# Optimization experiments

Hardware: AMD Instinct MI355X
Metric: run time of the kernel (lower is better)

## Reference

```python
import math
import jax, jax.numpy as jnp
import numpy as np

B, N, D = 64, 1024, 512


def setup_inputs() -> dict:
    key = jax.random.key(0)
    k1, k2, k3 = jax.random.split(key, 3)
    x = jax.random.normal(k1, (B, N, D), dtype=jnp.float32)
    # non-padded-elements mask: True = valid object (all valid here so every
    # softmax row has finite entries despite the -inf self-mask on the diagonal)
    mask = jnp.ones((B, N), dtype=bool)
    # fc_out = nn.Linear(D, D): weight [D, D] (out, in) and bias [D]
    lim = 1.0 / math.sqrt(D)
    W = jax.random.uniform(k2, (D, D), dtype=jnp.float32, minval=-lim, maxval=lim)
    b = jax.random.uniform(k3, (D,), dtype=jnp.float32, minval=-lim, maxval=lim)
    return {"x": x, "mask": mask, "W": W, "b": b}


def reference(x, mask, W, b):
    bsz, max_objs, embed_dim = x.shape
    xs = x / math.sqrt(embed_dim)  # note: values are the scaled x too (as in torch code)
    # sims[b, i, j] = <xs[b,i], xs[b,j]>
    sims = jnp.einsum('bid,bjd->bij', xs, xs)
    # mask padded KEYS (columns): ~mask -> -inf
    sims = jnp.where(mask[:, None, :], sims, -jnp.inf)
    # self-exclusion: eye(N).fill_diagonal_(-inf) == -inf on diag, 0 off-diag
    self_mask = jnp.where(jnp.eye(max_objs, dtype=bool), -jnp.inf, 0.0).astype(sims.dtype)
    sims = sims + self_mask
    attn_weights = jax.nn.softmax(sims, axis=-1)
    attn = jnp.einsum('bij,bjd->bid', attn_weights, xs)
    out = attn @ W.T + b
    return out
```

## Files before the change

kernel.cpp:

```cpp
#include <hip/hip_runtime.h>
#include <hip/hip_bf16.h>
#include <cstdint>
#include <cstddef>


typedef float f32x4 __attribute__((ext_vector_type(4)));
typedef unsigned short ushort4v __attribute__((ext_vector_type(4)));
typedef long longx2 __attribute__((ext_vector_type(2)));

#if __has_builtin(__builtin_amdgcn_cvt_pk_fp8_f32)
static __device__ __forceinline__ unsigned pk4_fp8(float a, float b, float c,
                                                   float d) {
  unsigned u = (unsigned)__builtin_amdgcn_cvt_pk_fp8_f32(a, b, 0, false);
  u = (unsigned)__builtin_amdgcn_cvt_pk_fp8_f32(c, d, (int)u, true);
  return u;
}
#else
static __device__ __forceinline__ unsigned f2e4m3_sw(float f) {
  unsigned s = (__float_as_uint(f) >> 24) & 0x80u;
  float a = fabsf(f);
  if (a != a) return s | 0x7fu;
  if (a > 448.f) a = 448.f;
  if (a == 0.f) return s;
  int e;
  float m = frexpf(a, &e);
  if (e - 1 < -6) {
    unsigned q = (unsigned)rintf(a * 512.f);
    return s | q;
  }
  unsigned q = (unsigned)rintf(m * 16.f);
  if (q == 16u) { q = 8u; e += 1; }
  return s | ((unsigned)(e - 1 + 7) << 3) | (q - 8u);
}
static __device__ __forceinline__ unsigned pk4_fp8(float a, float b, float c,
                                                   float d) {
  return f2e4m3_sw(a) | (f2e4m3_sw(b) << 8) | (f2e4m3_sw(c) << 16) |
         (f2e4m3_sw(d) << 24);
}
#endif

static __device__ __forceinline__ int perm8(int k) {
  return (k & ~127) | (k & 64) | (((k >> 3) & 3) << 4) |
         (((k >> 5) & 1) << 3) | (k & 7);
}

#define GLDS16(src, dst)                                                        \
  __builtin_amdgcn_global_load_lds(                                             \
      (const __attribute__((address_space(1))) void*)(src),                     \
      (__attribute__((address_space(3))) void*)(dst), 16, 0, 0)

__global__ __launch_bounds__(256) void convert_kernel(
    const float* __restrict__ x, unsigned char* __restrict__ xf8,
    unsigned char* __restrict__ xT8, const float* __restrict__ W,
    unsigned char* __restrict__ W8) {
  const int bid = blockIdx.x;
  const int t = threadIdx.x;
  if (bid >= 8192) {
    const int f0 = ((bid - 8192) * 256 + t) * 4;
    const int row = f0 >> 9, col = f0 & 511;
    const float4 v = *(const float4*)(W + f0);
    const unsigned u =
        pk4_fp8(v.x * 8.f, v.y * 8.f, v.z * 8.f, v.w * 8.f);
    *(unsigned*)(W8 + (size_t)row * 512 + perm8(col)) = u;
    return;
  }
  const int b = bid >> 7;
  const int tile = bid & 127;
  const int n0 = (tile >> 3) * 64;
  const int d0 = (tile & 7) * 64;
  __shared__ unsigned char T8[64][80];
  const float sc = 0.04419417382415922f;
  const size_t xbase = ((size_t)b * 1024 + n0) * 512 + d0;
#pragma unroll
  for (int q = 0; q < 2; ++q) {
    const int u = q * 256 + t;
    const int r = u >> 3, j = u & 7;
    const float4 v0 = *(const float4*)(x + xbase + (size_t)r * 512 + j * 8);
    const float4 v1 = *(const float4*)(x + xbase + (size_t)r * 512 + j * 8 + 4);
    const unsigned lo = pk4_fp8(v0.x * sc, v0.y * sc, v0.z * sc, v0.w * sc);
    const unsigned hi = pk4_fp8(v1.x * sc, v1.y * sc, v1.z * sc, v1.w * sc);
    const unsigned long long pk =
        (unsigned long long)lo | ((unsigned long long)hi << 32);
    const int k = d0 + j * 8;
    *(unsigned long long*)(xf8 + ((size_t)b * 1024 + n0 + r) * 512 +
                           perm8(k)) = pk;
    *(unsigned long long*)(&T8[r][j * 8]) = pk;
  }
  __syncthreads();
  const int dd = t >> 2;
  const int nc0 = (t & 3) * 16;
  unsigned long long lo = 0, hi = 0;
#pragma unroll
  for (int j = 0; j < 8; ++j) {
    lo |= (unsigned long long)T8[nc0 + j][dd] << (8 * j);
    hi |= (unsigned long long)T8[nc0 + 8 + j][dd] << (8 * j);
  }
  const size_t rowb = ((size_t)b * 512 + d0 + dd) * 1024;
  const int gn0 = n0 + nc0;
  *(unsigned long long*)(xT8 + rowb + perm8(gn0)) = lo;
  *(unsigned long long*)(xT8 + rowb + perm8(gn0 + 8)) = hi;
}

__global__ __launch_bounds__(256) void rsum_reduce_kernel(
    const float* __restrict__ part, float* __restrict__ invr) {
  const int i = blockIdx.x * 256 + threadIdx.x;
  const int b = i >> 10, row = i & 1023;
  const float* p = part + (size_t)b * 16384 + row;
  float s = 0.0f;
#pragma unroll
  for (int j = 0; j < 16; ++j) s += p[j * 1024];
  invr[i] = 1.0f / s;
}

template <int KB, int MODE, bool TRI>
__global__ __launch_bounds__(512, 4) void g128_kernel(
    const unsigned char* __restrict__ A, const unsigned char* __restrict__ Bm,
    void* __restrict__ Out, float* __restrict__ aux, int mB, int nB,
    size_t aBatch, size_t bBatch, size_t oBatch, int aStride, int bStride,
    int oStride) {
  __shared__ __align__(16) unsigned char lds[73728];

  const int nwg = gridDim.x;
  int bid = blockIdx.x;
  {
    const int xcd = bid & 7, loc = bid >> 3;
    const int q = nwg >> 3, r8 = nwg & 7;
    bid = (xcd < r8 ? xcd * (q + 1) : r8 * (q + 1) + (xcd - r8) * q) + loc;
  }
  int pb, mb, nb;
  if (TRI) {
    pb = bid / 20;
    int r = bid - pb * 20;
    mb = 0;
    while (r >= 8 - 2 * mb) { r -= 8 - 2 * mb; ++mb; }
    nb = 2 * mb + r;
  } else {
    const int per = mB * nB;
    pb = bid / per;
    const int rem = bid - pb * per;
    mb = rem / nB;
    nb = rem - mb * nB;
  }

  const int t = threadIdx.x;
  const int lane = t & 63;
  const int w = t >> 6;
  const int wm = w >> 1;
  const int wn = w & 1;
  const int g = lane >> 4, cc = lane & 15;

  const unsigned char* Ab =
      A + (size_t)pb * aBatch + (size_t)(mb * 256) * aStride;
  const unsigned char* Bb =
      Bm + (size_t)pb * bBatch + (size_t)(nb * 128) * bStride;

  const int rowS = t >> 2;
  const int swc = (((t & 3) ^ ((rowS >> 1) & 3)) << 4);

  auto stageA = [&](int slot, int half, int kt) {
    const unsigned char* src =
        Ab + (size_t)(half * 128 + rowS) * aStride + kt * 64 + swc;
    GLDS16(src, lds + slot * 16384 + half * 8192 + t * 16);
  };
  auto stageB = [&](int slot, int kt) {
    const unsigned char* src = Bb + (size_t)rowS * bStride + kt * 64 + swc;
    GLDS16(src, lds + 49152 + slot * 8192 + t * 16);
  };

  const int swz = ((g ^ ((cc >> 1) & 3)) << 4);
  const int aBase = wm * 4096 + cc * 64 + swz;
  const int bBase = wn * 4096 + cc * 64 + swz;

  f32x4 acc[4][4];
#pragma unroll
  for (int mt = 0; mt < 4; ++mt)
#pragma unroll
    for (int nt = 0; nt < 4; ++nt) acc[mt][nt] = 0.0f;

  longx2 af[4], bv[4];

  auto readAf = [&](int slot) {
#pragma unroll
    for (int j = 0; j < 4; ++j)
      af[j] = *reinterpret_cast<const longx2*>(lds + slot * 16384 + aBase +
                                               j * 1024);
  };
  auto readBf = [&](int slot) {
#pragma unroll
    for (int n = 0; n < 4; ++n)
      bv[n] = *reinterpret_cast<const longx2*>(lds + 49152 + slot * 8192 +
                                               bBase + n * 1024);
  };
  auto mfmaH = [&](int nh) {
    __builtin_amdgcn_s_setprio(1);
#pragma unroll
    for (int j = 0; j < 4; ++j)
#pragma unroll
      for (int n = 0; n < 2; ++n) {
        acc[j][nh * 2 + n] = __builtin_amdgcn_mfma_f32_16x16x32_fp8_fp8(
            bv[nh * 2 + n][0], af[j][0], acc[j][nh * 2 + n], 0, 0, 0);
        acc[j][nh * 2 + n] = __builtin_amdgcn_mfma_f32_16x16x32_fp8_fp8(
            bv[nh * 2 + n][1], af[j][1], acc[j][nh * 2 + n], 0, 0, 0);
      }
    __builtin_amdgcn_s_setprio(0);
  };

  stageA(0, 0, 0);
  stageA(0, 1, 0);
  stageB(0, 0);
  stageA(1, 0, 1);
  stageA(1, 1, 1);
  stageB(1, 1);
  asm volatile("s_waitcnt vmcnt(3)" ::: "memory");
  __builtin_amdgcn_s_barrier();

  int sl = 0;
#pragma unroll 1
  for (int kt = 0; kt < KB; ++kt) {
    const int s2 = (sl >= 1) ? sl - 1 : 2;
    const bool pf = (kt + 2 < KB);
    readAf(sl);
    readBf(sl);
    if (pf) {
      stageA(s2, 0, kt + 2);
      stageA(s2, 1, kt + 2);
      stageB(s2, kt + 2);
    }
    mfmaH(0);
    mfmaH(1);
    if (pf)
      asm volatile("s_waitcnt vmcnt(3)" ::: "memory");
    else
      asm volatile("s_waitcnt vmcnt(0)" ::: "memory");
    __builtin_amdgcn_s_barrier();
    sl = (sl == 2) ? 0 : sl + 1;
  }

  if (MODE == 0) {
    unsigned char* P = (unsigned char*)Out + (size_t)pb * oBatch;
    const bool mir = TRI && (nb >= 2 * mb + 2);
    float rs[4];
    float cs[4][4];
#pragma unroll
    for (int mt = 0; mt < 4; ++mt) rs[mt] = 0.0f;
#pragma unroll
    for (int nt = 0; nt < 4; ++nt)
#pragma unroll
      for (int r = 0; r < 4; ++r) cs[nt][r] = 0.0f;
#pragma unroll
    for (int mt = 0; mt < 4; ++mt) {
      const int ml = wm * 64 + mt * 16 + cc;
      const int mm = mb * 256 + ml;
#pragma unroll
      for (int nt = 0; nt < 4; ++nt) {
        const int cb = nb * 128 + wn * 64 + nt * 16 + g * 4;
        float p[4];
#pragma unroll
        for (int r = 0; r < 4; ++r) {
          p[r] = (mm == cb + r) ? 0.0f : __expf(acc[mt][nt][r]);
          rs[mt] += p[r];
        }
        const unsigned u = pk4_fp8(p[0], p[1], p[2], p[3]);
        *(unsigned*)(P + (size_t)mm * oStride + perm8(cb)) = u;
        if (mir) {
#pragma unroll
          for (int r = 0; r < 4; ++r) {
            const int nl = wn * 64 + nt * 16 + g * 4 + r;
            lds[nl * 256 + (ml ^ ((nl & 7) << 4))] =
                (unsigned char)(u >> (8 * r));
            cs[nt][r] += p[r];
          }
        }
      }
    }
#pragma unroll
    for (int mt = 0; mt < 4; ++mt) {
      rs[mt] += __shfl_xor(rs[mt], 16);
      rs[mt] += __shfl_xor(rs[mt], 32);
    }
    if (lane < 16) {
      const int sm = TRI ? (nb - 2 * mb) * 2 + wn : nb * 2 + wn;
      float* prt = aux + ((size_t)pb * 16 + sm) * 1024;
#pragma unroll
      for (int mt = 0; mt < 4; ++mt)
        prt[mb * 256 + wm * 64 + mt * 16 + lane] = rs[mt];
    }
    if (mir) {
#pragma unroll
      for (int nt = 0; nt < 4; ++nt)
#pragma unroll
        for (int r = 0; r < 4; ++r) {
          float v = cs[nt][r];
          v += __shfl_xor(v, 1);
          v += __shfl_xor(v, 2);
          v += __shfl_xor(v, 4);
          v += __shfl_xor(v, 8);
          if (cc == 0) {
            const int n = wn * 64 + nt * 16 + g * 4 + r;
            aux[((size_t)pb * 16 + (12 - 4 * mb + wm)) * 1024 + nb * 128 +
                n] = v;
          }
        }
      __syncthreads();
      const int nl = t >> 2, q4 = t & 3;
      const int swn = (nl & 7) << 4;
      unsigned char* Pm =
          P + (size_t)(nb * 128 + nl) * oStride + mb * 256;
#pragma unroll
      for (int c = 0; c < 4; ++c) {
        const int mc = q4 * 64 + c * 16;
        const unsigned long long* src =
            (const unsigned long long*)(lds + nl * 256 + (mc ^ swn));
        const unsigned long long q0 = src[0], q1 = src[1];
        *(unsigned long long*)(Pm + perm8(mc)) = q0;
        *(unsigned long long*)(Pm + perm8(mc + 8)) = q1;
      }
    }
  } else if (MODE == 1) {
    unsigned char* Ao = (unsigned char*)Out + (size_t)pb * oBatch;
    const float* invr = aux;
#pragma unroll
    for (int mt = 0; mt < 4; ++mt) {
      const int mm = mb * 256 + wm * 64 + mt * 16 + cc;
      const float inv = invr[(size_t)pb * 1024 + mm] * 256.0f;
#pragma unroll
      for (int nt = 0; nt < 4; ++nt) {
        const int nn = nb * 128 + wn * 64 + nt * 16 + g * 4;
        *(unsigned*)(Ao + (size_t)mm * oStride + perm8(nn)) =
            pk4_fp8(acc[mt][nt][0] * inv, acc[mt][nt][1] * inv,
                    acc[mt][nt][2] * inv, acc[mt][nt][3] * inv);
      }
    }
  } else {
    float* O = (float*)Out;
    const float* bias = (const float*)aux;
    const float is = 1.0f / 2048.0f;
#pragma unroll
    for (int mt = 0; mt < 4; ++mt) {
      const int mm = mb * 256 + wm * 64 + mt * 16 + cc;
#pragma unroll
      for (int nt = 0; nt < 4; ++nt) {
        const int nn = nb * 128 + wn * 64 + nt * 16 + g * 4;
        const float4 bv4 = *(const float4*)(bias + nn);
        float4 o;
        o.x = acc[mt][nt][0] * is + bv4.x;
        o.y = acc[mt][nt][1] * is + bv4.y;
        o.z = acc[mt][nt][2] * is + bv4.z;
        o.w = acc[mt][nt][3] * is + bv4.w;
        *(float4*)(O + (size_t)mm * oStride + nn) = o;
      }
    }
  }
}

extern "C" void kernel_launch(void* const* d_in, const int* in_sizes, int n_in,
                              void* d_out, int out_size, void* d_ws,
                              size_t ws_size, hipStream_t stream) {
  (void)in_sizes; (void)n_in; (void)out_size; (void)ws_size;
  const float* x = (const float*)d_in[0];
  const float* W = (const float*)d_in[2];
  const float* bias = (const float*)d_in[3];

  unsigned char* base = (unsigned char*)d_ws;
  unsigned char* xf8 = base;
  unsigned char* xT8 = base + 33554432ULL;
  unsigned char* attn8 = base + 67108864ULL;
  unsigned char* W8 = base + 100663296ULL;
  float* part = (float*)(base + 100925440ULL);
  float* invr = (float*)(base + 109314048ULL);
  unsigned char* P = base + 109576192ULL;

  convert_kernel<<<8448, 256, 0, stream>>>(x, xf8, xT8, W, W8);

  g128_kernel<8, 0, true><<<1280, 512, 0, stream>>>(
      xf8, xf8, P, part, 4, 8, 524288, 524288, 1048576, 512, 512, 1024);
  rsum_reduce_kernel<<<256, 256, 0, stream>>>(part, invr);
  g128_kernel<16, 1, false><<<1024, 512, 0, stream>>>(
      P, xT8, attn8, invr, 4, 4, 1048576, 524288, 524288, 1024, 1024, 512);
  g128_kernel<8, 2, false><<<1024, 512, 0, stream>>>(
      attn8, W8, d_out, (float*)bias, 256, 4, 0, 0, 0, 512, 512, 512);
}
```

Before: 204.3 us.

## Use smaller 128x128 tile kernel with 3-stage pipeline for PV and projection GEMMs

Adds a new g128c_kernel that computes 128x128 output tiles with 256 threads, a triple-buffered LDS pipeline, and launch bounds allowing 3 blocks per CU. The PV GEMM and the output projection now launch 2048 of these smaller blocks in place of 1024 blocks of 256x128. The original kernel keeps only the similarity mode. The aim is more blocks in flight and better latency hiding, at the cost of less data reuse per tile and more global traffic.

```diff
diff --git a/kernel.cpp b/kernel.cpp
--- a/kernel.cpp
+++ b/kernel.cpp
@@ -279,7 +279,7 @@
       rs[mt] += __shfl_xor(rs[mt], 32);
     }
     if (lane < 16) {
-      const int sm = TRI ? (nb - 2 * mb) * 2 + wn : nb * 2 + wn;
+      const int sm = (nb - 2 * mb) * 2 + wn;
       float* prt = aux + ((size_t)pb * 16 + sm) * 1024;
 #pragma unroll
       for (int mt = 0; mt < 4; ++mt)
@@ -316,12 +316,134 @@
         *(unsigned long long*)(Pm + perm8(mc + 8)) = q1;
       }
     }
-  } else if (MODE == 1) {
+  }
+}
+
+template <int KB, int MODE>
+__global__ __launch_bounds__(256, 3) void g128c_kernel(
+    const unsigned char* __restrict__ A, const unsigned char* __restrict__ Bm,
+    void* __restrict__ Out, float* __restrict__ aux, int mB, int nB,
+    size_t aBatch, size_t bBatch, size_t oBatch, int aStride, int bStride,
+    int oStride) {
+  __shared__ __align__(16) unsigned char lds[49152];
+
+  const int nwg = gridDim.x;
+  int bid = blockIdx.x;
+  {
+    const int xcd = bid & 7, loc = bid >> 3;
+    const int q = nwg >> 3, r8 = nwg & 7;
+    bid = (xcd < r8 ? xcd * (q + 1) : r8 * (q + 1) + (xcd - r8) * q) + loc;
+  }
+  const int per = mB * nB;
+  const int pb = bid / per;
+  const int rem = bid - pb * per;
+  const int mb = rem / nB;
+  const int nb = rem - mb * nB;
+
+  const int t = threadIdx.x;
+  const int lane = t & 63;
+  const int w = t >> 6;
+  const int wm = w >> 1;
+  const int wn = w & 1;
+  const int g = lane >> 4, cc = lane & 15;
+
+  const unsigned char* Ab =
+      A + (size_t)pb * aBatch + (size_t)(mb * 128) * aStride;
+  const unsigned char* Bb =
+      Bm + (size_t)pb * bBatch + (size_t)(nb * 128) * bStride;
+
+  const int rowS = t >> 2;
+  const int swc = (((t & 3) ^ ((rowS >> 1) & 3)) << 4);
+
+  auto stageA = [&](int slot, int kt) {
+#pragma unroll
+    for (int u = 0; u < 2; ++u) {
+      const unsigned char* src =
+          Ab + (size_t)(u * 64 + rowS) * aStride + kt * 64 + swc;
+      GLDS16(src, lds + slot * 8192 + u * 4096 + t * 16);
+    }
+  };
+  auto stageB = [&](int slot, int kt) {
+#pragma unroll
+    for (int u = 0; u < 2; ++u) {
+      const unsigned char* src =
+          Bb + (size_t)(u * 64 + rowS) * bStride + kt * 64 + swc;
+      GLDS16(src, lds + 24576 + slot * 8192 + u * 4096 + t * 16);
+    }
+  };
+
+  const int swz = ((g ^ ((cc >> 1) & 3)) << 4);
+  const int aBase = wm * 4096 + cc * 64 + swz;
+  const int bBase = wn * 4096 + cc * 64 + swz;
+
+  f32x4 acc[4][4];
+#pragma unroll
+  for (int mt = 0; mt < 4; ++mt)
+#pragma unroll
+    for (int nt = 0; nt < 4; ++nt) acc[mt][nt] = 0.0f;
+
+  longx2 af[4], bv[4];
+
+  auto readAf = [&](int slot) {
+#pragma unroll
+    for (int j = 0; j < 4; ++j)
+      af[j] = *reinterpret_cast<const longx2*>(lds + slot * 8192 + aBase +
+                                               j * 1024);
+  };
+  auto readBf = [&](int slot) {
+#pragma unroll
+    for (int n = 0; n < 4; ++n)
+      bv[n] = *reinterpret_cast<const longx2*>(lds + 24576 + slot * 8192 +
+                                               bBase + n * 1024);
+  };
+  auto mfmaH = [&](int nh) {
+    __builtin_amdgcn_s_setprio(1);
+#pragma unroll
+    for (int j = 0; j < 4; ++j)
+#pragma unroll
+      for (int n = 0; n < 2; ++n) {
+        acc[j][nh * 2 + n] = __builtin_amdgcn_mfma_f32_16x16x32_fp8_fp8(
+            bv[nh * 2 + n][0], af[j][0], acc[j][nh * 2 + n], 0, 0, 0);
+        acc[j][nh * 2 + n] = __builtin_amdgcn_mfma_f32_16x16x32_fp8_fp8(
+            bv[nh * 2 + n][1], af[j][1], acc[j][nh * 2 + n], 0, 0, 0);
+      }
+    __builtin_amdgcn_s_setprio(0);
+  };
+
+  stageA(0, 0);
+  stageB(0, 0);
+  stageA(1, 1);
+  stageB(1, 1);
+  asm volatile("s_waitcnt vmcnt(4)" ::: "memory");
+  __builtin_amdgcn_s_barrier();
+
+  int sl = 0;
+#pragma unroll 1
+  for (int kt = 0; kt < KB; ++kt) {
+    const int s2 = (sl >= 1) ? sl - 1 : 2;
+    const bool pf = (kt + 2 < KB);
+    readAf(sl);
+    readBf(sl);
+    if (pf) {
+      stageA(s2, kt + 2);
+      stageB(s2, kt + 2);
+    }
+    mfmaH(0);
+    mfmaH(1);
+    if (pf)
+      asm volatile("s_waitcnt vmcnt(4)" ::: "memory");
+    else
+      asm volatile("s_waitcnt vmcnt(0)" ::: "memory");
+    __builtin_amdgcn_s_barrier();
+    sl = (sl == 2) ? 0 : sl + 1;
+  }
+
+  if (MODE == 1) {
     unsigned char* Ao = (unsigned char*)Out + (size_t)pb * oBatch;
     const float* invr = aux;
 #pragma unroll
     for (int mt = 0; mt < 4; ++mt) {
-      const int mm = mb * 256 + wm * 64 + mt * 16 + cc;
+      const int mm = mb * 128 + wm * 64 + mt * 16 + cc;
       const float inv = invr[(size_t)pb * 1024 + mm] * 256.0f;
 #pragma unroll
       for (int nt = 0; nt < 4; ++nt) {
@@ -337,7 +459,7 @@
     const float is = 1.0f / 2048.0f;
 #pragma unroll
     for (int mt = 0; mt < 4; ++mt) {
-      const int mm = mb * 256 + wm * 64 + mt * 16 + cc;
+      const int mm = mb * 128 + wm * 64 + mt * 16 + cc;
 #pragma unroll
       for (int nt = 0; nt < 4; ++nt) {
         const int nn = nb * 128 + wn * 64 + nt * 16 + g * 4;
@@ -375,8 +497,8 @@
   g128_kernel<8, 0, true><<<1280, 512, 0, stream>>>(
       xf8, xf8, P, part, 4, 8, 524288, 524288, 1048576, 512, 512, 1024);
   rsum_reduce_kernel<<<256, 256, 0, stream>>>(part, invr);
-  g128_kernel<16, 1, false><<<1024, 512, 0, stream>>>(
-      P, xT8, attn8, invr, 4, 4, 1048576, 524288, 524288, 1024, 1024, 512);
-  g128_kernel<8, 2, false><<<1024, 512, 0, stream>>>(
-      attn8, W8, d_out, (float*)bias, 256, 4, 0, 0, 0, 512, 512, 512);
-}
+  g128c_kernel<16, 1><<<2048, 256, 0, stream>>>(
+      P, xT8, attn8, invr, 8, 4, 1048576, 524288, 524288, 1024, 1024, 512);
+  g128c_kernel<8, 2><<<2048, 256, 0, stream>>>(
+      attn8, W8, d_out, (float*)bias, 512, 4, 0, 0, 0, 512, 512, 512);
+}
```

After: 204.8 us. About the same (+0.3%).
